# Optimization experiments

Measured on AMD Instinct MI355X. Metric: run time of the kernel, lower is better.

## Reference

```python
import jax, jax.numpy as jnp
import numpy as np

B, T, D = 8, 1024, 1024
DMAX = 8
MAX_FRAMES = T * DMAX  # static upper bound on expanded length
SPEED = 1.0
EPS = 1e-5


def setup_inputs() -> dict:
    key = jax.random.key(0)
    ks = jax.random.split(key, 8)
    s = 0.02
    return {
        "x": jax.random.normal(ks[0], (B, T, D), dtype=jnp.float32),
        "target_durations": jax.random.randint(ks[1], (B, T), 0, DMAX, dtype=jnp.int32),
        "w1": jax.random.normal(ks[2], (D, D, 3), dtype=jnp.float32) * s,
        "b1": jnp.zeros((D,), jnp.float32),
        "g1": jnp.ones((D,), jnp.float32),
        "be1": jnp.zeros((D,), jnp.float32),
        "w2": jax.random.normal(ks[3], (D, D, 3), dtype=jnp.float32) * s,
        "b2": jnp.zeros((D,), jnp.float32),
        "g2": jnp.ones((D,), jnp.float32),
        "be2": jnp.zeros((D,), jnp.float32),
        "wl": jax.random.normal(ks[4], (1, D), dtype=jnp.float32) * s,
        "bl": jnp.zeros((1,), jnp.float32),
    }


def _conv1d(h, w, b):
    # h: [B, C, T], w: [O, I, K], padding=1 (same)
    o = jax.lax.conv_general_dilated(h, w, window_strides=(1,), padding=((1, 1),),
                                     dimension_numbers=("NCH", "OIH", "NCH"))
    return o + b[None, :, None]


def _ln(h, g, b):
    # layernorm over last dim
    m = jnp.mean(h, axis=-1, keepdims=True)
    v = jnp.mean(jnp.square(h - m), axis=-1, keepdims=True)
    return (h - m) * jax.lax.rsqrt(v + EPS) * g + b


def _predictor(x, w1, b1, g1, be1, w2, b2, g2, be2, wl, bl):
    h = jnp.transpose(x, (0, 2, 1))                  # [B, D, T]
    h = jax.nn.relu(_conv1d(h, w1, b1))
    h = _ln(jnp.transpose(h, (0, 2, 1)), g1, be1)    # [B, T, D]
    h = jnp.transpose(h, (0, 2, 1))
    h = jax.nn.relu(_conv1d(h, w2, b2))
    h = _ln(jnp.transpose(h, (0, 2, 1)), g2, be2)    # [B, T, D]
    return (h @ wl.T + bl)[..., 0]                   # [B, T] log-durations


def _expand(x, durations):
    # vectorized length regulation: token index per output frame via searchsorted
    cum = jnp.cumsum(durations, axis=1)              # [B, T]
    frames = jnp.arange(MAX_FRAMES)                  # [F]
    tok = jax.vmap(lambda c: jnp.searchsorted(c, frames, side="right"))(cum)  # [B, F]
    valid = frames[None, :] < cum[:, -1:]            # [B, F]
    tok = jnp.minimum(tok, x.shape[1] - 1)
    out = jnp.take_along_axis(x, tok[:, :, None], axis=1)  # [B, F, D]
    return jnp.where(valid[:, :, None], out, 0.0)


def reference(x, target_durations, w1, b1, g1, be1, w2, b2, g2, be2, wl, bl):
    log_d = _predictor(x, w1, b1, g1, be1, w2, b2, g2, be2, wl, bl)
    _pred = jnp.maximum(jnp.round(jnp.exp(log_d) / SPEED).astype(jnp.int32), 1)
    durations = target_durations  # target path overrides prediction
    padded = _expand(x, durations)
    return padded, durations
```

## Files before the change

### kernel.cpp

```cpp
#include <hip/hip_runtime.h>


#define B_ 8
#define T_ 1024
#define D_ 1024
#define F_ 8192

__global__ void __launch_bounds__(1024) dur_scan_kernel(
    const int* __restrict__ dur,
    int* __restrict__ tok_map,
    float* __restrict__ out_dur)
{
    __shared__ int s[T_];
    const int b = blockIdx.x;
    const int t = threadIdx.x;

    const int d = dur[b * T_ + t];
    out_dur[b * T_ + t] = (float)d;

    s[t] = d;
    __syncthreads();
    #pragma unroll
    for (int off = 1; off < T_; off <<= 1) {
        int v = (t >= off) ? s[t - off] : 0;
        __syncthreads();
        s[t] += v;
        __syncthreads();
    }

    const int cum_t    = s[t];
    const int cum_prev = (t > 0) ? s[t - 1] : 0;
    const int total    = s[T_ - 1];

    int* tm = tok_map + b * F_;
    for (int f = cum_prev; f < cum_t; ++f) tm[f] = t;
    for (int f = total + t; f < F_; f += T_) tm[f] = -1;
}

__global__ void __launch_bounds__(256) expand_kernel(
    const float* __restrict__ x,
    const int* __restrict__ tok_map,
    float* __restrict__ out)
{
    const int bf  = blockIdx.x;
    const int b   = bf >> 13;
    const int tok = tok_map[bf];

    float4* dst = reinterpret_cast<float4*>(out)
                + (size_t)bf * (D_ / 4) + threadIdx.x;
    if (tok < 0) {
        *dst = make_float4(0.f, 0.f, 0.f, 0.f);
    } else {
        const float4* src = reinterpret_cast<const float4*>(x)
                          + ((size_t)b * T_ + (size_t)tok) * (D_ / 4) + threadIdx.x;
        *dst = *src;
    }
}

extern "C" void kernel_launch(void* const* d_in, const int* in_sizes, int n_in,
                              void* d_out, int out_size, void* d_ws, size_t ws_size,
                              hipStream_t stream)
{
    const float* x   = (const float*)d_in[0];
    const int*   dur = (const int*)d_in[1];

    float* out     = (float*)d_out;
    float* out_dur = out + (size_t)B_ * F_ * D_;
    int*   tok_map = (int*)d_ws;

    dur_scan_kernel<<<B_, T_, 0, stream>>>(dur, tok_map, out_dur);
    expand_kernel<<<B_ * F_, 256, 0, stream>>>(x, tok_map, out);
}
```

Before: 326.9 us.

## Replace gather-per-frame with scatter-per-token plus separate tail zero-fill

The scan kernel now writes only cumulative durations instead of a per-frame token map. A new scatter kernel has one block per input token read its row once and write it to each output frame it covers. A separate kernel zero-fills frames past the total length in chunks of 32 rows. This drops the frame-map writes and the repeated source reads, but adds a third launch and leaves blocks idle when a token's duration is zero.

```diff
diff --git a/kernel.cpp b/kernel.cpp
--- a/kernel.cpp
+++ b/kernel.cpp
@@ -5,10 +5,14 @@
 #define T_ 1024
 #define D_ 1024
 #define F_ 8192
+#define DV4 (D_ / 4)
+#define ZROWS 32
+
+typedef float vfloat4 __attribute__((ext_vector_type(4)));
 
 __global__ void __launch_bounds__(1024) dur_scan_kernel(
     const int* __restrict__ dur,
-    int* __restrict__ tok_map,
+    int* __restrict__ cum,
     float* __restrict__ out_dur)
 {
     __shared__ int s[T_];
@@ -27,33 +31,45 @@
         s[t] += v;
         __syncthreads();
     }
-
-    const int cum_t    = s[t];
-    const int cum_prev = (t > 0) ? s[t - 1] : 0;
-    const int total    = s[T_ - 1];
-
-    int* tm = tok_map + b * F_;
-    for (int f = cum_prev; f < cum_t; ++f) tm[f] = t;
-    for (int f = total + t; f < F_; f += T_) tm[f] = -1;
+    cum[b * T_ + t] = s[t];
 }
 
-__global__ void __launch_bounds__(256) expand_kernel(
+__global__ void __launch_bounds__(256) scatter_kernel(
     const float* __restrict__ x,
-    const int* __restrict__ tok_map,
+    const int* __restrict__ cum,
     float* __restrict__ out)
 {
-    const int bf  = blockIdx.x;
-    const int b   = bf >> 13;
-    const int tok = tok_map[bf];
+    const int bt = blockIdx.x;
+    const int b  = bt >> 10;
+    const int t  = bt & (T_ - 1);
 
-    float4* dst = reinterpret_cast<float4*>(out)
-                + (size_t)bf * (D_ / 4) + threadIdx.x;
-    if (tok < 0) {
-        *dst = make_float4(0.f, 0.f, 0.f, 0.f);
-    } else {
-        const float4* src = reinterpret_cast<const float4*>(x)
-                          + ((size_t)b * T_ + (size_t)tok) * (D_ / 4) + threadIdx.x;
-        *dst = *src;
+    const int c1 = cum[bt];
+    const int c0 = t ? cum[bt - 1] : 0;
+    if (c0 == c1) return;
+
+    const vfloat4 v = reinterpret_cast<const vfloat4*>(x)[(size_t)bt * DV4 + threadIdx.x];
+    vfloat4* dstb = reinterpret_cast<vfloat4*>(out)
+                  + (size_t)b * F_ * DV4 + threadIdx.x;
+    for (int r = c0; r < c1; ++r)
+        dstb[(size_t)r * DV4] = v;
+}
+
+__global__ void __launch_bounds__(256) zerofill_kernel(
+    const int* __restrict__ cum,
+    float* __restrict__ out)
+{
+    const int chunk = blockIdx.x * ZROWS;
+    const int b     = chunk >> 13;
+    const int f0    = chunk & (F_ - 1);
+    const int total = cum[b * T_ + T_ - 1];
+    if (f0 + ZROWS <= total) return;
+
+    vfloat4* dstb = reinterpret_cast<vfloat4*>(out)
+                  + (size_t)chunk * DV4 + threadIdx.x;
+    #pragma unroll 4
+    for (int r = 0; r < ZROWS; ++r) {
+        if (f0 + r >= total)
+            dstb[(size_t)r * DV4] = (vfloat4)(0.f);
     }
 }
 
@@ -66,8 +82,9 @@
 
     float* out     = (float*)d_out;
     float* out_dur = out + (size_t)B_ * F_ * D_;
-    int*   tok_map = (int*)d_ws;
+    int*   cum     = (int*)d_ws;
 
-    dur_scan_kernel<<<B_, T_, 0, stream>>>(dur, tok_map, out_dur);
-    expand_kernel<<<B_ * F_, 256, 0, stream>>>(x, tok_map, out);
+    dur_scan_kernel<<<B_, T_, 0, stream>>>(dur, cum, out_dur);
+    scatter_kernel<<<B_ * T_, 256, 0, stream>>>(x, cum, out);
+    zerofill_kernel<<<(B_ * F_) / ZROWS, 256, 0, stream>>>(cum, out);
 }
```

New measurement: 325.3 us. No clear change (-0.5%).
